# Kernel tuning notes

Hardware: AMD Instinct MI355X
Metric: run time of the kernel (lower is better)

Reference implementation:

```python
import jax, jax.numpy as jnp
import numpy as np

NUM_SAMPLED = 512       # num_sampled_points
EXTRA_WIDTH = 1.0       # pool_extra_width


def setup_inputs() -> dict:
    key = jax.random.key(0)
    k1, k2, k3, k4, k5, k6 = jax.random.split(key, 6)
    B, N, C, M = 4, 16384, 128, 128
    # lidar-like points: xy in [0,40] m, z in [-2,2] m
    xy = jax.random.uniform(k1, (B, N, 2), jnp.float32, 0.0, 40.0)
    z = jax.random.uniform(k2, (B, N, 1), jnp.float32, -2.0, 2.0)
    points = jnp.concatenate([xy, z], axis=-1)
    point_features = jax.random.normal(k3, (B, N, C), jnp.float32)
    # boxes: centers in same range, dims 1-5 m, heading in [-pi, pi]
    cxy = jax.random.uniform(k4, (B, M, 2), jnp.float32, 0.0, 40.0)
    cz = jax.random.uniform(k5, (B, M, 1), jnp.float32, -1.0, 1.0)
    dims = jax.random.uniform(k6, (B, M, 3), jnp.float32, 1.0, 5.0)
    heading = jax.random.uniform(jax.random.fold_in(key, 7), (B, M, 1), jnp.float32, -3.14159, 3.14159)
    boxes3d = jnp.concatenate([cxy, cz, dims, heading], axis=-1)
    return {"points": points, "point_features": point_features, "boxes3d": boxes3d}


def _pool_one(points, feats, boxes):
    # points (N,3), feats (N,C), boxes (M,7)
    N = points.shape[0]
    center = boxes[:, 0:3]                      # (M,3)
    dims = boxes[:, 3:6] + 2.0 * EXTRA_WIDTH    # enlarge_box3d: dx,dy,dz += 2*extra
    heading = boxes[:, 6]                       # (M,)
    # shift into box-centered frame: (M,N)
    sx = points[None, :, 0] - center[:, 0:1]
    sy = points[None, :, 1] - center[:, 1:2]
    sz = points[None, :, 2] - center[:, 2:3]
    ch = jnp.cos(heading)[:, None]
    sh = jnp.sin(heading)[:, None]
    # rotate by -heading into box local frame
    lx = sx * ch + sy * sh
    ly = -sx * sh + sy * ch
    mask = (jnp.abs(lx) < dims[:, 0:1] * 0.5) \
         & (jnp.abs(ly) < dims[:, 1:2] * 0.5) \
         & (jnp.abs(sz) < dims[:, 2:3] * 0.5)   # (M,N)
    cnt = mask.sum(axis=1)                       # (M,) points in each box
    # stable order of matched point indices: matched first, in original order
    order_key = jnp.where(mask, jnp.arange(N, dtype=jnp.int32)[None, :], N)
    idx_sorted = jnp.argsort(order_key, axis=1)[:, :NUM_SAMPLED]  # (M,S)
    # slot k takes the (k mod cnt)-th matched point (wrap-around duplication)
    k = jnp.arange(NUM_SAMPLED, dtype=jnp.int32)[None, :]
    cnt_safe = jnp.maximum(cnt, 1)[:, None]
    wrapped = k % cnt_safe                       # (M,S), k when cnt>k
    gather_idx = jnp.take_along_axis(idx_sorted, wrapped, axis=1)  # (M,S)
    data = jnp.concatenate([points, feats], axis=1)  # (N,3+C)
    pooled = data[gather_idx]                    # (M,S,3+C)
    empty = (cnt == 0).astype(jnp.int32)         # (M,)
    pooled = jnp.where(empty[:, None, None] > 0, jnp.zeros((), pooled.dtype), pooled)
    return pooled, empty


def reference(points, point_features, boxes3d):
    pooled_features, pooled_empty_flag = jax.vmap(_pool_one)(points, point_features, boxes3d)
    return pooled_features, pooled_empty_flag
```

## Files before the change

### kernel.cpp

```cpp
#include <hip/hip_runtime.h>

#define BATCH 4
#define NPTS 16384
#define NBOX 128
#define NFEAT 128
#define NS 512
#define ROW 131
#define NWORDS (NPTS / 64)
#define ROWS_PER_BLK 32
#define SUBS (NS / ROWS_PER_BLK)

__global__ __launch_bounds__(256) void mask_kernel(
    const float* __restrict__ points,
    const float* __restrict__ boxes,
    unsigned short* __restrict__ gi_ws,
    int* __restrict__ cnt_ws,
    float* __restrict__ out_flag)
{
#pragma clang fp contract(off)
    const int box_id = blockIdx.x;
    const int b      = box_id >> 7;
    const int tid    = threadIdx.x;
    const int wave   = tid >> 6;
    const int lane   = tid & 63;

    __shared__ unsigned long long s_bits[NWORDS];
    __shared__ int s_idx[NS];
    __shared__ int s_wsum[4];

    const float* bx = boxes + box_id * 7;
    const float cx = bx[0], cy = bx[1], cz = bx[2];
    const float hx = bx[3] * 0.5f + 1.0f;
    const float hy = bx[4] * 0.5f + 1.0f;
    const float hz = bx[5] * 0.5f + 1.0f;
    const double hd = (double)bx[6];
    const float ch = (float)cos(hd);
    const float sh = (float)sin(hd);

    const float* pts = points + (size_t)b * NPTS * 3;

    for (int it = 0; it < NPTS / 256; ++it) {
        const int i = it * 256 + wave * 64 + lane;
        const float px = pts[i * 3 + 0];
        const float py = pts[i * 3 + 1];
        const float pz = pts[i * 3 + 2];
        const float sx = px - cx;
        const float sy = py - cy;
        const float sz = pz - cz;
        const float t0 = sx * ch;
        const float t1 = sy * sh;
        const float lx = t0 + t1;
        const float t2 = (-sx) * sh;
        const float t3 = sy * ch;
        const float ly = t2 + t3;
        const bool inside = (fabsf(lx) < hx) && (fabsf(ly) < hy) && (fabsf(sz) < hz);
        const unsigned long long m = __ballot(inside);
        if (lane == 0) s_bits[it * 4 + wave] = m;
    }
    __syncthreads();

    const unsigned long long w = s_bits[tid];
    const int pc = __popcll(w);
    int pre = pc;
    #pragma unroll
    for (int off = 1; off < 64; off <<= 1) {
        const int v = __shfl_up(pre, off);
        if (lane >= off) pre += v;
    }
    if (lane == 63) s_wsum[wave] = pre;
    __syncthreads();
    int wbase = 0;
    for (int i = 0; i < wave; ++i) wbase += s_wsum[i];
    const int total = s_wsum[0] + s_wsum[1] + s_wsum[2] + s_wsum[3];
    int pos = wbase + (pre - pc);
    unsigned long long mm = w;
    while (mm && pos < NS) {
        const int bit = __builtin_ctzll(mm);
        s_idx[pos] = tid * 64 + bit;
        ++pos;
        mm &= (mm - 1);
    }
    const int cnt = (total < NS) ? total : NS;
    __syncthreads();

    if (tid == 0) {
        cnt_ws[box_id] = cnt;
        out_flag[box_id] = (cnt == 0) ? 1.0f : 0.0f;
    }
    if (cnt > 0) {
        for (int k = tid; k < NS; k += 256) {
            const int j = (k < cnt) ? k : (k % cnt);
            gi_ws[box_id * NS + k] = (unsigned short)s_idx[j];
        }
    }
}

__global__ __launch_bounds__(256) void gather_kernel(
    const float* __restrict__ points,
    const float* __restrict__ feats,
    const unsigned short* __restrict__ gi_ws,
    const int* __restrict__ cnt_ws,
    float* __restrict__ out_pooled)
{
    const int blk    = blockIdx.x;
    const int box_id = blk >> 4;
    const int sub    = blk & (SUBS - 1);
    const int b      = box_id >> 7;
    const int tid    = threadIdx.x;
    const int wave   = tid >> 6;
    const int lane   = tid & 63;

    __shared__ float s_row[ROWS_PER_BLK * ROW];
    __shared__ unsigned short s_gi[ROWS_PER_BLK];

    const int cnt = cnt_ws[box_id];
    float* outg = out_pooled + (size_t)blk * (ROWS_PER_BLK * ROW);

    if (cnt == 0) {
        float4 z = make_float4(0.f, 0.f, 0.f, 0.f);
        float4* og = (float4*)outg;
        for (int i = tid; i < (ROWS_PER_BLK * ROW) / 4; i += 256) og[i] = z;
        return;
    }

    if (tid < ROWS_PER_BLK) s_gi[tid] = gi_ws[box_id * NS + sub * ROWS_PER_BLK + tid];
    __syncthreads();

    const float* pts = points + (size_t)b * NPTS * 3;
    const float* fb  = feats  + (size_t)b * NPTS * NFEAT;

    const int cg = lane & 31;
    const int rh = lane >> 5;
    #pragma unroll
    for (int it = 0; it < 4; ++it) {
        const int row = wave * 8 + it * 2 + rh;
        const int gi  = s_gi[row];
        const float4 f = *(const float4*)(fb + (size_t)gi * NFEAT + cg * 4);
        float* sr = s_row + row * ROW;
        sr[3 + cg * 4 + 0] = f.x;
        sr[3 + cg * 4 + 1] = f.y;
        sr[3 + cg * 4 + 2] = f.z;
        sr[3 + cg * 4 + 3] = f.w;
        if (cg < 3) sr[cg] = pts[gi * 3 + cg];
    }
    __syncthreads();

    const float4* sv = (const float4*)s_row;
    float4* og = (float4*)outg;
    for (int i = tid; i < (ROWS_PER_BLK * ROW) / 4; i += 256) og[i] = sv[i];
}

extern "C" void kernel_launch(void* const* d_in, const int* in_sizes, int n_in,
                              void* d_out, int out_size, void* d_ws, size_t ws_size,
                              hipStream_t stream) {
    const float* points = (const float*)d_in[0];
    const float* feats  = (const float*)d_in[1];
    const float* boxes  = (const float*)d_in[2];
    float* out_pooled = (float*)d_out;
    float* out_flag   = out_pooled + (size_t)BATCH * NBOX * NS * ROW;

    unsigned short* gi_ws = (unsigned short*)d_ws;
    int* cnt_ws = (int*)(gi_ws + (size_t)BATCH * NBOX * NS);

    mask_kernel<<<BATCH * NBOX, 256, 0, stream>>>(points, boxes, gi_ws, cnt_ws, out_flag);
    gather_kernel<<<BATCH * NBOX * SUBS, 256, 0, stream>>>(points, feats, gi_ws, cnt_ws, out_pooled);
}
```

Before: 212.1 us.

## Split ballot over point quarters and fold compaction into gather blocks

The mask pass now runs four blocks per box, each covering a quarter of the points and writing ballot bitmasks to a global workspace. The prefix-sum compaction and the wrap-around index selection move into the gather kernel, which each of the 16 sub-blocks per box recomputes from the bitmask. This is meant to raise parallelism in the first kernel, which had only 512 blocks each looping over all points. The cost is compaction work repeated 16 times per box, plus extra shared memory in the gather kernel.

```diff
diff --git a/kernel.cpp b/kernel.cpp
--- a/kernel.cpp
+++ b/kernel.cpp
@@ -7,26 +7,23 @@
 #define NS 512
 #define ROW 131
 #define NWORDS (NPTS / 64)
+#define QCHUNK 4096
 #define ROWS_PER_BLK 32
 #define SUBS (NS / ROWS_PER_BLK)
 
-__global__ __launch_bounds__(256) void mask_kernel(
+__global__ __launch_bounds__(256) void ballot_kernel(
     const float* __restrict__ points,
     const float* __restrict__ boxes,
-    unsigned short* __restrict__ gi_ws,
-    int* __restrict__ cnt_ws,
-    float* __restrict__ out_flag)
+    unsigned long long* __restrict__ bits_ws)
 {
 #pragma clang fp contract(off)
-    const int box_id = blockIdx.x;
+    const int blk    = blockIdx.x;
+    const int box_id = blk >> 2;
+    const int q      = blk & 3;
     const int b      = box_id >> 7;
     const int tid    = threadIdx.x;
     const int wave   = tid >> 6;
     const int lane   = tid & 63;
-
-    __shared__ unsigned long long s_bits[NWORDS];
-    __shared__ int s_idx[NS];
-    __shared__ int s_wsum[4];
 
     const float* bx = boxes + box_id * 7;
     const float cx = bx[0], cy = bx[1], cz = bx[2];
@@ -38,9 +35,11 @@
     const float sh = (float)sin(hd);
 
     const float* pts = points + (size_t)b * NPTS * 3;
+    unsigned long long* bw = bits_ws + (size_t)box_id * NWORDS + q * (QCHUNK / 64);
 
-    for (int it = 0; it < NPTS / 256; ++it) {
-        const int i = it * 256 + wave * 64 + lane;
+    #pragma unroll 4
+    for (int it = 0; it < QCHUNK / 256; ++it) {
+        const int i = q * QCHUNK + it * 256 + wave * 64 + lane;
         const float px = pts[i * 3 + 0];
         const float py = pts[i * 3 + 1];
         const float pz = pts[i * 3 + 2];
@@ -55,11 +54,31 @@
         const float ly = t2 + t3;
         const bool inside = (fabsf(lx) < hx) && (fabsf(ly) < hy) && (fabsf(sz) < hz);
         const unsigned long long m = __ballot(inside);
-        if (lane == 0) s_bits[it * 4 + wave] = m;
+        if (lane == 0) bw[it * 4 + wave] = m;
     }
-    __syncthreads();
+}
 
-    const unsigned long long w = s_bits[tid];
+__global__ __launch_bounds__(256) void pool_kernel(
+    const float* __restrict__ points,
+    const float* __restrict__ feats,
+    const unsigned long long* __restrict__ bits_ws,
+    float* __restrict__ out_pooled,
+    float* __restrict__ out_flag)
+{
+    const int blk    = blockIdx.x;
+    const int box_id = blk >> 4;
+    const int sub    = blk & (SUBS - 1);
+    const int b      = box_id >> 7;
+    const int tid    = threadIdx.x;
+    const int wave   = tid >> 6;
+    const int lane   = tid & 63;
+
+    __shared__ int s_idx[NS];
+    __shared__ int s_gi[ROWS_PER_BLK];
+    __shared__ int s_wsum[4];
+    __shared__ float s_row[ROWS_PER_BLK * ROW];
+
+    const unsigned long long w = bits_ws[(size_t)box_id * NWORDS + tid];
     const int pc = __popcll(w);
     int pre = pc;
     #pragma unroll
@@ -83,37 +102,8 @@
     const int cnt = (total < NS) ? total : NS;
     __syncthreads();
 
-    if (tid == 0) {
-        cnt_ws[box_id] = cnt;
-        out_flag[box_id] = (cnt == 0) ? 1.0f : 0.0f;
-    }
-    if (cnt > 0) {
-        for (int k = tid; k < NS; k += 256) {
-            const int j = (k < cnt) ? k : (k % cnt);
-            gi_ws[box_id * NS + k] = (unsigned short)s_idx[j];
-        }
-    }
-}
+    if (sub == 0 && tid == 0) out_flag[box_id] = (cnt == 0) ? 1.0f : 0.0f;
 
-__global__ __launch_bounds__(256) void gather_kernel(
-    const float* __restrict__ points,
-    const float* __restrict__ feats,
-    const unsigned short* __restrict__ gi_ws,
-    const int* __restrict__ cnt_ws,
-    float* __restrict__ out_pooled)
-{
-    const int blk    = blockIdx.x;
-    const int box_id = blk >> 4;
-    const int sub    = blk & (SUBS - 1);
-    const int b      = box_id >> 7;
-    const int tid    = threadIdx.x;
-    const int wave   = tid >> 6;
-    const int lane   = tid & 63;
-
-    __shared__ float s_row[ROWS_PER_BLK * ROW];
-    __shared__ unsigned short s_gi[ROWS_PER_BLK];
-
-    const int cnt = cnt_ws[box_id];
     float* outg = out_pooled + (size_t)blk * (ROWS_PER_BLK * ROW);
 
     if (cnt == 0) {
@@ -123,7 +113,11 @@
         return;
     }
 
-    if (tid < ROWS_PER_BLK) s_gi[tid] = gi_ws[box_id * NS + sub * ROWS_PER_BLK + tid];
+    if (tid < ROWS_PER_BLK) {
+        const int k = sub * ROWS_PER_BLK + tid;
+        const int j = (k < cnt) ? k : (k % cnt);
+        s_gi[tid] = s_idx[j];
+    }
     __syncthreads();
 
     const float* pts = points + (size_t)b * NPTS * 3;
@@ -159,9 +153,9 @@
     float* out_pooled = (float*)d_out;
     float* out_flag   = out_pooled + (size_t)BATCH * NBOX * NS * ROW;
 
-    unsigned short* gi_ws = (unsigned short*)d_ws;
-    int* cnt_ws = (int*)(gi_ws + (size_t)BATCH * NBOX * NS);
+    unsigned long long* bits_ws = (unsigned long long*)d_ws;
 
-    mask_kernel<<<BATCH * NBOX, 256, 0, stream>>>(points, boxes, gi_ws, cnt_ws, out_flag);
-    gather_kernel<<<BATCH * NBOX * SUBS, 256, 0, stream>>>(points, feats, gi_ws, cnt_ws, out_pooled);
+    ballot_kernel<<<BATCH * NBOX * 4, 256, 0, stream>>>(points, boxes, bits_ws);
+    pool_kernel<<<BATCH * NBOX * SUBS, 256, 0, stream>>>(points, feats, bits_ws,
+                                                         out_pooled, out_flag);
 }
```

After: 190.7 us. 10.1% less time.
